# Performance work log

Measured on AMD Instinct MI355X. Metric: run time of the kernel, lower is better.

The kernel has to match this reference:

```python
import jax, jax.numpy as jnp
import numpy as np

N_NODES = 50000


def gcn_conv(h_in, W, b, src, dst, deg_inv_sqrt):
    """PyG GCNConv with self-loops and symmetric normalization.
    out_i = sum_{j->i} d_j^{-1/2} d_i^{-1/2} (h_j W) + d_i^{-1} (h_i W) + b
    """
    h = h_in @ W  # [N, out] transform first (efficient GCN form)
    norm = deg_inv_sqrt[src] * deg_inv_sqrt[dst]  # [E]
    msg = h[src] * norm[:, None]  # [E, out] edge gather
    agg = jax.ops.segment_sum(msg, dst, num_segments=N_NODES)
    # self-loop contribution with norm d_i^{-1/2} * d_i^{-1/2}
    agg = agg + h * (deg_inv_sqrt ** 2)[:, None]
    return agg + b


def setup_inputs() -> dict:
    key = jax.random.key(0)
    ks = jax.random.split(key, 8)
    n_input, n_hidden, n_latent = 512, 96, 32
    E = 800000
    x = jax.random.normal(ks[0], (N_NODES, n_input), dtype=jnp.float32)
    edge_index = jax.random.randint(ks[1], (2, E), 0, N_NODES, dtype=jnp.int64)
    s = 0.05
    W1 = jax.random.normal(ks[2], (n_input, n_hidden), dtype=jnp.float32) * s
    b1 = jnp.zeros((n_hidden,), dtype=jnp.float32)
    W_mu = jax.random.normal(ks[3], (n_hidden, n_latent), dtype=jnp.float32) * s
    b_mu = jnp.zeros((n_latent,), dtype=jnp.float32)
    W_logstd = jax.random.normal(ks[4], (n_hidden, n_latent), dtype=jnp.float32) * s
    b_logstd = jnp.zeros((n_latent,), dtype=jnp.float32)
    return {"x": x, "W1": W1, "b1": b1, "W_mu": W_mu, "b_mu": b_mu,
            "W_logstd": W_logstd, "b_logstd": b_logstd, "edge_index": edge_index}


def reference(x, W1, b1, W_mu, b_mu, W_logstd, b_logstd, edge_index):
    src, dst = edge_index[0], edge_index[1]
    # degree from targets with self-loops (PyG gcn_norm convention)
    deg = jax.ops.segment_sum(jnp.ones_like(dst, dtype=x.dtype), dst,
                              num_segments=N_NODES) + 1.0
    deg_inv_sqrt = jax.lax.rsqrt(deg)
    hidden = jax.nn.relu(gcn_conv(x, W1, b1, src, dst, deg_inv_sqrt))
    # dropout_rate = 0.0 -> identity
    mu = gcn_conv(hidden, W_mu, b_mu, src, dst, deg_inv_sqrt)
    logstd = gcn_conv(hidden, W_logstd, b_logstd, src, dst, deg_inv_sqrt)
    return (mu, logstd)
```

## Files before the change

### kernel.cpp

```cpp
#include <hip/hip_runtime.h>
#include <hip/hip_bf16.h>

#define N_NODES 50000
#define NIN 512
#define NH 96
#define NL 32
#define NH2 64

#define NB2 196
#define NBLK 128
#define BCAP 5120

typedef __attribute__((ext_vector_type(8))) short short8v;
typedef __attribute__((ext_vector_type(4))) float f32x4;

__device__ __forceinline__ unsigned short f2bf(float f) {
    __hip_bfloat16 h = __float2bfloat16(f);
    unsigned short u;
    __builtin_memcpy(&u, &h, 2);
    return u;
}
__device__ __forceinline__ float bf2f(unsigned short h) {
    return __uint_as_float((unsigned)h << 16);
}

__global__ __launch_bounds__(256) void k_prep(const float* __restrict__ W1,
                                              const float* __restrict__ Wmu,
                                              const float* __restrict__ Wls,
                                              unsigned short* __restrict__ WbT,
                                              unsigned short* __restrict__ W2T,
                                              int* __restrict__ gcur) {
    int idx = blockIdx.x * 256 + threadIdx.x;
    if (idx < NH * NIN) {
        int n = idx >> 9, k = idx & 511;
        WbT[idx] = f2bf(W1[(size_t)k * NH + n]);
    } else if (idx < NH * NIN + NH2 * NH) {
        int j = idx - NH * NIN;
        int n = j / NH, k = j - n * NH;
        float v = (n < NL) ? Wmu[k * NL + n] : Wls[k * NL + (n - NL)];
        W2T[j] = f2bf(v);
    }
    if (idx < NB2) gcur[idx] = 0;
}

__global__ __launch_bounds__(256) void k_coarse(const int* __restrict__ src,
                                                const int* __restrict__ dst,
                                                int* __restrict__ gcur,
                                                unsigned* __restrict__ cpair, int E) {
    __shared__ int hist[NB2];
    __shared__ int lpos[NB2];
    int t = threadIdx.x;
    int ch = (E + NBLK - 1) / NBLK;
    int e0 = blockIdx.x * ch, e1 = min(e0 + ch, E);
    for (int b = t; b < NB2; b += 256) hist[b] = 0;
    __syncthreads();
    for (int e = e0 + t; e < e1; e += 256)
        atomicAdd(&hist[dst[e] >> 8], 1);
    __syncthreads();
    for (int b = t; b < NB2; b += 256) {
        int cnt = hist[b];
        int base = (cnt > 0) ? atomicAdd(&gcur[b], cnt) : 0;
        lpos[b] = b * BCAP + base;
    }
    __syncthreads();
    for (int e = e0 + t; e < e1; e += 256) {
        int s = src[e], d = dst[e];
        int pos = atomicAdd(&lpos[d >> 8], 1);
        cpair[pos] = (unsigned)s | ((unsigned)d << 16);
    }
}

__global__ __launch_bounds__(256) void k_fine(const unsigned* __restrict__ cpair,
                                              const int* __restrict__ gcur,
                                              int* __restrict__ rowoff,
                                              float* __restrict__ dis,
                                              int* __restrict__ esrc) {
    __shared__ int lcnt[256];
    __shared__ int lscan[256];
    int bb = blockIdx.x;
    int n0 = bb << 8;
    int t = threadIdx.x;
    lscan[t] = (t < bb) ? gcur[t] : 0;
    __syncthreads();
    for (int off = 128; off > 0; off >>= 1) {
        if (t < off) lscan[t] += lscan[t + off];
        __syncthreads();
    }
    int base = lscan[0];
    if (bb == NB2 - 1 && t == 0) rowoff[N_NODES] = base + gcur[bb];
    lcnt[t] = 0;
    __syncthreads();
    int p0 = bb * BCAP;
    int p1 = p0 + gcur[bb];
    for (int p = p0 + t; p < p1; p += 256)
        atomicAdd(&lcnt[(cpair[p] >> 16) - n0], 1);
    __syncthreads();
    int cnt = lcnt[t];
    lscan[t] = cnt;
    __syncthreads();
    for (int off = 1; off < 256; off <<= 1) {
        int u = (t >= off) ? lscan[t - off] : 0;
        __syncthreads();
        lscan[t] += u;
        __syncthreads();
    }
    int excl = lscan[t] - cnt;
    int node = n0 + t;
    if (node < N_NODES) {
        rowoff[node] = base + excl;
        dis[node] = rsqrtf((float)cnt + 1.0f);
    }
    lcnt[t] = base + excl;
    __syncthreads();
    for (int p = p0 + t; p < p1; p += 256) {
        unsigned u = cpair[p];
        int d = (int)(u >> 16);
        int pos = atomicAdd(&lcnt[d - n0], 1);
        esrc[pos] = (int)(u & 0xFFFFu);
    }
}

#define GBM 64
__global__ __launch_bounds__(256, 3) void k_gemm1(const float* __restrict__ x,
                                                  const unsigned short* __restrict__ WbT,
                                                  const float* __restrict__ dis,
                                                  unsigned short* __restrict__ hb, int M) {
    __shared__ __align__(16) char lA[64 * 128];
    __shared__ __align__(16) char lB[96 * 128];
    int tid = threadIdx.x;
    int lane = tid & 63, w = tid >> 6;
    int l15 = lane & 15, hi = lane >> 4;
    int m0 = blockIdx.x * GBM;

    f32x4 acc[6];
#pragma unroll
    for (int nt = 0; nt < 6; ++nt)
#pragma unroll
        for (int i = 0; i < 4; ++i) acc[nt][i] = 0.f;

    int key = l15 & 7;
    int arow = (w * 16 + l15) * 128;

    for (int kt = 0; kt < 8; ++kt) {
        __syncthreads();
#pragma unroll
        for (int i = 0; i < 2; ++i) {
            int s = i * 256 + tid;
            int r = s >> 3, sl = s & 7;
            const float* p = x + (size_t)min(m0 + r, M - 1) * NIN + kt * 64 + sl * 8;
            float4 a0 = *reinterpret_cast<const float4*>(p);
            float4 a1 = *reinterpret_cast<const float4*>(p + 4);
            uint4 pk;
            pk.x = (unsigned)f2bf(a0.x) | ((unsigned)f2bf(a0.y) << 16);
            pk.y = (unsigned)f2bf(a0.z) | ((unsigned)f2bf(a0.w) << 16);
            pk.z = (unsigned)f2bf(a1.x) | ((unsigned)f2bf(a1.y) << 16);
            pk.w = (unsigned)f2bf(a1.z) | ((unsigned)f2bf(a1.w) << 16);
            *reinterpret_cast<uint4*>(lA + r * 128 + ((sl ^ (r & 7)) << 4)) = pk;
        }
#pragma unroll
        for (int i = 0; i < 3; ++i) {
            int s = i * 256 + tid;
            int n = s >> 3, sl = s & 7;
            uint4 bv = *reinterpret_cast<const uint4*>(WbT + (size_t)n * NIN + kt * 64 + sl * 8);
            *reinterpret_cast<uint4*>(lB + n * 128 + ((sl ^ (n & 7)) << 4)) = bv;
        }
        __syncthreads();

#pragma unroll
        for (int kc = 0; kc < 2; ++kc) {
            int off = (((kc * 4 + hi) ^ key) << 4);
            short8v a = *reinterpret_cast<const short8v*>(lA + arow + off);
#pragma unroll
            for (int nt = 0; nt < 6; ++nt) {
                short8v bv = *reinterpret_cast<const short8v*>(lB + (nt * 16 + l15) * 128 + off);
                acc[nt] = __builtin_amdgcn_mfma_f32_16x16x32_bf16(a, bv, acc[nt], 0, 0, 0);
            }
        }
    }

    int rbase = m0 + w * 16 + hi * 4;
#pragma unroll
    for (int r = 0; r < 4; ++r) {
        int orow = rbase + r;
        if (orow < M) {
            float dv = dis[orow];
            unsigned short* op = hb + (size_t)orow * NH + l15;
#pragma unroll
            for (int nt = 0; nt < 6; ++nt) op[nt * 16] = f2bf(acc[nt][r] * dv);
        }
    }
}

__global__ __launch_bounds__(256) void k_gather1(const ushort4* __restrict__ hb4,
                                                 const int* __restrict__ rowoff,
                                                 const int* __restrict__ esrc,
                                                 const float* __restrict__ dis,
                                                 const float* __restrict__ b1,
                                                 ushort4* __restrict__ hid4) {
    int tid = threadIdx.x;
    int node = blockIdx.x * 8 + (tid >> 5);
    int c = tid & 31;
    if (node >= N_NODES) return;
    int p0 = rowoff[node], p1 = rowoff[node + 1];
    bool act = (c < 24);
    float ax = 0.f, ay = 0.f, az = 0.f, aw = 0.f;
    for (int pb = p0; pb < p1; pb += 32) {
        int nb = min(32, p1 - pb);
        int sv = (c < nb) ? esrc[pb + c] : 0;
#pragma unroll 4
        for (int j = 0; j < nb; j++) {
            int s = __shfl(sv, j, 32);
            if (act) {
                ushort4 v = hb4[(size_t)s * 24 + c];
                ax += bf2f(v.x); ay += bf2f(v.y); az += bf2f(v.z); aw += bf2f(v.w);
            }
        }
    }
    if (act) {
        float dv = dis[node];
        ushort4 hv = hb4[(size_t)node * 24 + c];
        float4 bv = reinterpret_cast<const float4*>(b1)[c];
        ushort4 o;
        o.x = f2bf(fmaxf((ax + bf2f(hv.x)) * dv + bv.x, 0.f));
        o.y = f2bf(fmaxf((ay + bf2f(hv.y)) * dv + bv.y, 0.f));
        o.z = f2bf(fmaxf((az + bf2f(hv.z)) * dv + bv.z, 0.f));
        o.w = f2bf(fmaxf((aw + bf2f(hv.w)) * dv + bv.w, 0.f));
        hid4[(size_t)node * 24 + c] = o;
    }
}

#define GBM2 64
__global__ __launch_bounds__(256) void k_gemm2(const unsigned short* __restrict__ hid,
                                               const unsigned short* __restrict__ W2T,
                                               const float* __restrict__ dis,
                                               unsigned short* __restrict__ h23, int M) {
    __shared__ __align__(16) char lA[64 * 256];
    __shared__ __align__(16) char lB[64 * 256];
    int tid = threadIdx.x;
    int lane = tid & 63, w = tid >> 6;
    int l15 = lane & 15, hi = lane >> 4;
    int m0 = blockIdx.x * GBM2;

#pragma unroll
    for (int i = 0; i < 3; ++i) {
        int s = i * 256 + tid;
        int r = s / 12, sl = s - r * 12;
        uint4 v = *reinterpret_cast<const uint4*>(
            hid + (size_t)min(m0 + r, M - 1) * NH + sl * 8);
        *reinterpret_cast<uint4*>(lA + r * 256 + ((sl ^ (r & 7)) << 4)) = v;
    }
#pragma unroll
    for (int i = 0; i < 3; ++i) {
        int s = i * 256 + tid;
        int n = s / 12, sl = s - n * 12;
        uint4 v = *reinterpret_cast<const uint4*>(W2T + (size_t)n * NH + sl * 8);
        *reinterpret_cast<uint4*>(lB + n * 256 + ((sl ^ (n & 7)) << 4)) = v;
    }
    __syncthreads();

    f32x4 acc[4];
#pragma unroll
    for (int nt = 0; nt < 4; ++nt)
#pragma unroll
        for (int i = 0; i < 4; ++i) acc[nt][i] = 0.f;

    int key = l15 & 7;
    const char* aptr = lA + (w * 16 + l15) * 256;
#pragma unroll
    for (int kc = 0; kc < 3; ++kc) {
        int off = (((kc * 4 + hi) ^ key) << 4);
        short8v a = *reinterpret_cast<const short8v*>(aptr + off);
#pragma unroll
        for (int nt = 0; nt < 4; ++nt) {
            short8v bv = *reinterpret_cast<const short8v*>(lB + (nt * 16 + l15) * 256 + off);
            acc[nt] = __builtin_amdgcn_mfma_f32_16x16x32_bf16(a, bv, acc[nt], 0, 0, 0);
        }
    }

    int rbase = m0 + w * 16 + hi * 4;
#pragma unroll
    for (int r = 0; r < 4; ++r) {
        int orow = rbase + r;
        if (orow < M) {
            float dv = dis[orow];
            unsigned short* op = h23 + (size_t)orow * NH2 + l15;
#pragma unroll
            for (int nt = 0; nt < 4; ++nt) op[nt * 16] = f2bf(acc[nt][r] * dv);
        }
    }
}

__global__ __launch_bounds__(256) void k_gather2(const ushort4* __restrict__ hb4,
                                                 const int* __restrict__ rowoff,
                                                 const int* __restrict__ esrc,
                                                 const float* __restrict__ dis,
                                                 const float* __restrict__ bmu,
                                                 const float* __restrict__ bls,
                                                 float4* __restrict__ out4) {
    int tid = threadIdx.x;
    int node = blockIdx.x * 16 + (tid >> 4);
    int c = tid & 15;
    if (node >= N_NODES) return;
    int p0 = rowoff[node], p1 = rowoff[node + 1];
    float ax = 0.f, ay = 0.f, az = 0.f, aw = 0.f;
    for (int pb = p0; pb < p1; pb += 16) {
        int nb = min(16, p1 - pb);
        int sv = (c < nb) ? esrc[pb + c] : 0;
#pragma unroll 4
        for (int j = 0; j < nb; j++) {
            int s = __shfl(sv, j, 16);
            ushort4 v = hb4[(size_t)s * 16 + c];
            ax += bf2f(v.x); ay += bf2f(v.y); az += bf2f(v.z); aw += bf2f(v.w);
        }
    }
    float dv = dis[node];
    ushort4 hv = hb4[(size_t)node * 16 + c];
    float4 bv = (c < 8) ? reinterpret_cast<const float4*>(bmu)[c]
                        : reinterpret_cast<const float4*>(bls)[c - 8];
    float4 o;
    o.x = (ax + bf2f(hv.x)) * dv + bv.x;
    o.y = (ay + bf2f(hv.y)) * dv + bv.y;
    o.z = (az + bf2f(hv.z)) * dv + bv.z;
    o.w = (aw + bf2f(hv.w)) * dv + bv.w;
    if (c < 8) out4[(size_t)node * 8 + c] = o;
    else       out4[(size_t)N_NODES * 8 + (size_t)node * 8 + (c - 8)] = o;
}

extern "C" void kernel_launch(void* const* d_in, const int* in_sizes, int n_in,
                              void* d_out, int out_size, void* d_ws, size_t ws_size,
                              hipStream_t stream) {
    const float* x   = (const float*)d_in[0];
    const float* W1  = (const float*)d_in[1];
    const float* b1  = (const float*)d_in[2];
    const float* Wmu = (const float*)d_in[3];
    const float* bmu = (const float*)d_in[4];
    const float* Wls = (const float*)d_in[5];
    const float* bls = (const float*)d_in[6];
    const int*   ei  = (const int*)d_in[7];
    int E = in_sizes[7] / 2;
    const int* src  = ei;
    const int* dstp = ei + E;

    char* w = (char*)d_ws;
    int* rowoff  = (int*)w;            w += ((size_t)N_NODES + 4) * 4;
    float* dis   = (float*)w;          w += (size_t)N_NODES * 4;
    int* gcur    = (int*)w;            w += ((size_t)NB2 + 4) * 4;
    int* esrc    = (int*)w;            w += (size_t)E * 4;
    unsigned* cpair = (unsigned*)w;    w += (size_t)NB2 * BCAP * 4;
    unsigned short* WbT  = (unsigned short*)w;  w += (size_t)NH * NIN * 2;
    unsigned short* W2T  = (unsigned short*)w;  w += (size_t)NH2 * NH * 2;
    unsigned short* hbuf = (unsigned short*)w;  w += (size_t)N_NODES * NH * 2;
    unsigned short* hid  = (unsigned short*)w;  w += (size_t)N_NODES * NH * 2;
    unsigned short* h23  = (unsigned short*)w;  w += (size_t)N_NODES * NH2 * 2;

    int prep_n = NH * NIN + NH2 * NH;
    k_prep<<<(prep_n + 255) / 256, 256, 0, stream>>>(W1, Wmu, Wls, WbT, W2T, gcur);

    k_coarse<<<NBLK, 256, 0, stream>>>(src, dstp, gcur, cpair, E);
    k_fine<<<NB2, 256, 0, stream>>>(cpair, gcur, rowoff, dis, esrc);

    k_gemm1<<<(N_NODES + GBM - 1) / GBM, 256, 0, stream>>>(x, WbT, dis, hbuf, N_NODES);

    k_gather1<<<(N_NODES + 7) / 8, 256, 0, stream>>>(
        (const ushort4*)hbuf, rowoff, esrc, dis, b1, (ushort4*)hid);

    k_gemm2<<<(N_NODES + GBM2 - 1) / GBM2, 256, 0, stream>>>(hid, W2T, dis, h23, N_NODES);

    k_gather2<<<(N_NODES + 15) / 16, 256, 0, stream>>>(
        (const ushort4*)h23, rowoff, esrc, dis, bmu, bls, (float4*)d_out);
}
```

Before: 140.5 us.

## Widen gather loads to 16B, double GEMM1 K-tile, cache edges in LDS

Both gather kernels now load 8 bf16 values (uint4) per lane instead of 4, so fewer lanes serve each node and more nodes fit per block. GEMM1 processes K in 128-wide tiles over 4 iterations instead of 64-wide over 8, which halves the barrier count but doubles LDS use. The coarse bucketing kernel stages packed src/dst pairs in shared memory so the second pass does not re-read the edge arrays from global memory. These changes raise LDS pressure, which may lower occupancy in GEMM1 and k_coarse.

```diff
diff --git a/kernel.cpp b/kernel.cpp
--- a/kernel.cpp
+++ b/kernel.cpp
@@ -10,6 +10,7 @@
 #define NB2 196
 #define NBLK 128
 #define BCAP 5120
+#define ECH 6250
 
 typedef __attribute__((ext_vector_type(8))) short short8v;
 typedef __attribute__((ext_vector_type(4))) float f32x4;
@@ -20,6 +21,8 @@
     __builtin_memcpy(&u, &h, 2);
     return u;
 }
+__device__ __forceinline__ float bflo(unsigned u) { return __uint_as_float(u << 16); }
+__device__ __forceinline__ float bfhi(unsigned u) { return __uint_as_float(u & 0xFFFF0000u); }
 __device__ __forceinline__ float bf2f(unsigned short h) {
     return __uint_as_float((unsigned)h << 16);
 }
@@ -47,15 +50,20 @@
                                                 const int* __restrict__ dst,
                                                 int* __restrict__ gcur,
                                                 unsigned* __restrict__ cpair, int E) {
+    __shared__ unsigned epk[ECH];
     __shared__ int hist[NB2];
     __shared__ int lpos[NB2];
     int t = threadIdx.x;
     int ch = (E + NBLK - 1) / NBLK;
     int e0 = blockIdx.x * ch, e1 = min(e0 + ch, E);
+    int n = e1 - e0;
     for (int b = t; b < NB2; b += 256) hist[b] = 0;
     __syncthreads();
-    for (int e = e0 + t; e < e1; e += 256)
-        atomicAdd(&hist[dst[e] >> 8], 1);
+    for (int li = t; li < n; li += 256) {
+        int s = src[e0 + li], d = dst[e0 + li];
+        epk[li] = (unsigned)s | ((unsigned)d << 16);
+        atomicAdd(&hist[d >> 8], 1);
+    }
     __syncthreads();
     for (int b = t; b < NB2; b += 256) {
         int cnt = hist[b];
@@ -63,10 +71,10 @@
         lpos[b] = b * BCAP + base;
     }
     __syncthreads();
-    for (int e = e0 + t; e < e1; e += 256) {
-        int s = src[e], d = dst[e];
-        int pos = atomicAdd(&lpos[d >> 8], 1);
-        cpair[pos] = (unsigned)s | ((unsigned)d << 16);
+    for (int li = t; li < n; li += 256) {
+        unsigned u = epk[li];
+        int pos = atomicAdd(&lpos[u >> 24], 1);
+        cpair[pos] = u;
     }
 }
 
@@ -125,8 +133,8 @@
                                                   const unsigned short* __restrict__ WbT,
                                                   const float* __restrict__ dis,
                                                   unsigned short* __restrict__ hb, int M) {
-    __shared__ __align__(16) char lA[64 * 128];
-    __shared__ __align__(16) char lB[96 * 128];
+    __shared__ __align__(16) char lA[64 * 256];
+    __shared__ __align__(16) char lB[96 * 256];
     int tid = threadIdx.x;
     int lane = tid & 63, w = tid >> 6;
     int l15 = lane & 15, hi = lane >> 4;
@@ -139,15 +147,15 @@
         for (int i = 0; i < 4; ++i) acc[nt][i] = 0.f;
 
     int key = l15 & 7;
-    int arow = (w * 16 + l15) * 128;
-
-    for (int kt = 0; kt < 8; ++kt) {
+    int arow = (w * 16 + l15) * 256;
+
+    for (int kt = 0; kt < 4; ++kt) {
         __syncthreads();
 #pragma unroll
-        for (int i = 0; i < 2; ++i) {
+        for (int i = 0; i < 4; ++i) {
             int s = i * 256 + tid;
-            int r = s >> 3, sl = s & 7;
-            const float* p = x + (size_t)min(m0 + r, M - 1) * NIN + kt * 64 + sl * 8;
+            int r = s >> 4, sl = s & 15;
+            const float* p = x + (size_t)min(m0 + r, M - 1) * NIN + kt * 128 + sl * 8;
             float4 a0 = *reinterpret_cast<const float4*>(p);
             float4 a1 = *reinterpret_cast<const float4*>(p + 4);
             uint4 pk;
@@ -155,24 +163,24 @@
             pk.y = (unsigned)f2bf(a0.z) | ((unsigned)f2bf(a0.w) << 16);
             pk.z = (unsigned)f2bf(a1.x) | ((unsigned)f2bf(a1.y) << 16);
             pk.w = (unsigned)f2bf(a1.z) | ((unsigned)f2bf(a1.w) << 16);
-            *reinterpret_cast<uint4*>(lA + r * 128 + ((sl ^ (r & 7)) << 4)) = pk;
-        }
-#pragma unroll
-        for (int i = 0; i < 3; ++i) {
+            *reinterpret_cast<uint4*>(lA + r * 256 + ((sl ^ (r & 7)) << 4)) = pk;
+        }
+#pragma unroll
+        for (int i = 0; i < 6; ++i) {
             int s = i * 256 + tid;
-            int n = s >> 3, sl = s & 7;
-            uint4 bv = *reinterpret_cast<const uint4*>(WbT + (size_t)n * NIN + kt * 64 + sl * 8);
-            *reinterpret_cast<uint4*>(lB + n * 128 + ((sl ^ (n & 7)) << 4)) = bv;
+            int n = s >> 4, sl = s & 15;
+            uint4 bv = *reinterpret_cast<const uint4*>(WbT + (size_t)n * NIN + kt * 128 + sl * 8);
+            *reinterpret_cast<uint4*>(lB + n * 256 + ((sl ^ (n & 7)) << 4)) = bv;
         }
         __syncthreads();
 
 #pragma unroll
-        for (int kc = 0; kc < 2; ++kc) {
+        for (int kc = 0; kc < 4; ++kc) {
             int off = (((kc * 4 + hi) ^ key) << 4);
             short8v a = *reinterpret_cast<const short8v*>(lA + arow + off);
 #pragma unroll
             for (int nt = 0; nt < 6; ++nt) {
-                short8v bv = *reinterpret_cast<const short8v*>(lB + (nt * 16 + l15) * 128 + off);
+                short8v bv = *reinterpret_cast<const short8v*>(lB + (nt * 16 + l15) * 256 + off);
                 acc[nt] = __builtin_amdgcn_mfma_f32_16x16x32_bf16(a, bv, acc[nt], 0, 0, 0);
             }
         }
@@ -191,41 +199,54 @@
     }
 }
 
-__global__ __launch_bounds__(256) void k_gather1(const ushort4* __restrict__ hb4,
+__global__ __launch_bounds__(256) void k_gather1(const uint4* __restrict__ hb4,
                                                  const int* __restrict__ rowoff,
                                                  const int* __restrict__ esrc,
                                                  const float* __restrict__ dis,
                                                  const float* __restrict__ b1,
-                                                 ushort4* __restrict__ hid4) {
+                                                 uint4* __restrict__ hid4) {
     int tid = threadIdx.x;
-    int node = blockIdx.x * 8 + (tid >> 5);
-    int c = tid & 31;
+    int node = blockIdx.x * 16 + (tid >> 4);
+    int c = tid & 15;
     if (node >= N_NODES) return;
     int p0 = rowoff[node], p1 = rowoff[node + 1];
-    bool act = (c < 24);
-    float ax = 0.f, ay = 0.f, az = 0.f, aw = 0.f;
-    for (int pb = p0; pb < p1; pb += 32) {
-        int nb = min(32, p1 - pb);
+    bool act = (c < 12);
+    float a0 = 0.f, a1 = 0.f, a2 = 0.f, a3 = 0.f;
+    float a4 = 0.f, a5 = 0.f, a6 = 0.f, a7 = 0.f;
+    for (int pb = p0; pb < p1; pb += 16) {
+        int nb = min(16, p1 - pb);
         int sv = (c < nb) ? esrc[pb + c] : 0;
 #pragma unroll 4
         for (int j = 0; j < nb; j++) {
-            int s = __shfl(sv, j, 32);
+            int s = __shfl(sv, j, 16);
             if (act) {
-                ushort4 v = hb4[(size_t)s * 24 + c];
-                ax += bf2f(v.x); ay += bf2f(v.y); az += bf2f(v.z); aw += bf2f(v.w);
+                uint4 v = hb4[(size_t)s * 12 + c];
+                a0 += bflo(v.x); a1 += bfhi(v.x);
+                a2 += bflo(v.y); a3 += bfhi(v.y);
+                a4 += bflo(v.z); a5 += bfhi(v.z);
+                a6 += bflo(v.w); a7 += bfhi(v.w);
             }
         }
     }
     if (act) {
         float dv = dis[node];
-        ushort4 hv = hb4[(size_t)node * 24 + c];
-        float4 bv = reinterpret_cast<const float4*>(b1)[c];
-        ushort4 o;
-        o.x = f2bf(fmaxf((ax + bf2f(hv.x)) * dv + bv.x, 0.f));
-        o.y = f2bf(fmaxf((ay + bf2f(hv.y)) * dv + bv.y, 0.f));
-        o.z = f2bf(fmaxf((az + bf2f(hv.z)) * dv + bv.z, 0.f));
-        o.w = f2bf(fmaxf((aw + bf2f(hv.w)) * dv + bv.w, 0.f));
-        hid4[(size_t)node * 24 + c] = o;
+        uint4 hv = hb4[(size_t)node * 12 + c];
+        float4 b0 = reinterpret_cast<const float4*>(b1)[c * 2];
+        float4 b4 = reinterpret_cast<const float4*>(b1)[c * 2 + 1];
+        float r0 = fmaxf((a0 + bflo(hv.x)) * dv + b0.x, 0.f);
+        float r1 = fmaxf((a1 + bfhi(hv.x)) * dv + b0.y, 0.f);
+        float r2 = fmaxf((a2 + bflo(hv.y)) * dv + b0.z, 0.f);
+        float r3 = fmaxf((a3 + bfhi(hv.y)) * dv + b0.w, 0.f);
+        float r4 = fmaxf((a4 + bflo(hv.z)) * dv + b4.x, 0.f);
+        float r5 = fmaxf((a5 + bfhi(hv.z)) * dv + b4.y, 0.f);
+        float r6 = fmaxf((a6 + bflo(hv.w)) * dv + b4.z, 0.f);
+        float r7 = fmaxf((a7 + bfhi(hv.w)) * dv + b4.w, 0.f);
+        uint4 o;
+        o.x = (unsigned)f2bf(r0) | ((unsigned)f2bf(r1) << 16);
+        o.y = (unsigned)f2bf(r2) | ((unsigned)f2bf(r3) << 16);
+        o.z = (unsigned)f2bf(r4) | ((unsigned)f2bf(r5) << 16);
+        o.w = (unsigned)f2bf(r6) | ((unsigned)f2bf(r7) << 16);
+        hid4[(size_t)node * 12 + c] = o;
     }
 }
 
@@ -290,7 +311,7 @@
     }
 }
 
-__global__ __launch_bounds__(256) void k_gather2(const ushort4* __restrict__ hb4,
+__global__ __launch_bounds__(256) void k_gather2(const uint4* __restrict__ hb4,
                                                  const int* __restrict__ rowoff,
                                                  const int* __restrict__ esrc,
                                                  const float* __restrict__ dis,
@@ -298,32 +319,43 @@
                                                  const float* __restrict__ bls,
                                                  float4* __restrict__ out4) {
     int tid = threadIdx.x;
-    int node = blockIdx.x * 16 + (tid >> 4);
-    int c = tid & 15;
+    int node = blockIdx.x * 32 + (tid >> 3);
+    int c = tid & 7;
     if (node >= N_NODES) return;
     int p0 = rowoff[node], p1 = rowoff[node + 1];
-    float ax = 0.f, ay = 0.f, az = 0.f, aw = 0.f;
-    for (int pb = p0; pb < p1; pb += 16) {
-        int nb = min(16, p1 - pb);
+    float a0 = 0.f, a1 = 0.f, a2 = 0.f, a3 = 0.f;
+    float a4 = 0.f, a5 = 0.f, a6 = 0.f, a7 = 0.f;
+    for (int pb = p0; pb < p1; pb += 8) {
+        int nb = min(8, p1 - pb);
         int sv = (c < nb) ? esrc[pb + c] : 0;
 #pragma unroll 4
         for (int j = 0; j < nb; j++) {
-            int s = __shfl(sv, j, 16);
-            ushort4 v = hb4[(size_t)s * 16 + c];
-            ax += bf2f(v.x); ay += bf2f(v.y); az += bf2f(v.z); aw += bf2f(v.w);
+            int s = __shfl(sv, j, 8);
+            uint4 v = hb4[(size_t)s * 8 + c];
+            a0 += bflo(v.x); a1 += bfhi(v.x);
+            a2 += bflo(v.y); a3 += bfhi(v.y);
+            a4 += bflo(v.z); a5 += bfhi(v.z);
+            a6 += bflo(v.w); a7 += bfhi(v.w);
         }
     }
     float dv = dis[node];
-    ushort4 hv = hb4[(size_t)node * 16 + c];
-    float4 bv = (c < 8) ? reinterpret_cast<const float4*>(bmu)[c]
-                        : reinterpret_cast<const float4*>(bls)[c - 8];
-    float4 o;
-    o.x = (ax + bf2f(hv.x)) * dv + bv.x;
-    o.y = (ay + bf2f(hv.y)) * dv + bv.y;
-    o.z = (az + bf2f(hv.z)) * dv + bv.z;
-    o.w = (aw + bf2f(hv.w)) * dv + bv.w;
-    if (c < 8) out4[(size_t)node * 8 + c] = o;
-    else       out4[(size_t)N_NODES * 8 + (size_t)node * 8 + (c - 8)] = o;
+    uint4 hv = hb4[(size_t)node * 8 + c];
+    const float4* bp = (c < 4) ? reinterpret_cast<const float4*>(bmu) + c * 2
+                               : reinterpret_cast<const float4*>(bls) + (c - 4) * 2;
+    float4 b0 = bp[0], b4 = bp[1];
+    float4 o0, o1;
+    o0.x = (a0 + bflo(hv.x)) * dv + b0.x;
+    o0.y = (a1 + bfhi(hv.x)) * dv + b0.y;
+    o0.z = (a2 + bflo(hv.y)) * dv + b0.z;
+    o0.w = (a3 + bfhi(hv.y)) * dv + b0.w;
+    o1.x = (a4 + bflo(hv.z)) * dv + b4.x;
+    o1.y = (a5 + bfhi(hv.z)) * dv + b4.y;
+    o1.z = (a6 + bflo(hv.w)) * dv + b4.z;
+    o1.w = (a7 + bfhi(hv.w)) * dv + b4.w;
+    size_t base = (c < 4) ? (size_t)node * 8 + c * 2
+                          : (size_t)N_NODES * 8 + (size_t)node * 8 + (c - 4) * 2;
+    out4[base] = o0;
+    out4[base + 1] = o1;
 }
 
 extern "C" void kernel_launch(void* const* d_in, const int* in_sizes, int n_in,
@@ -361,11 +393,11 @@
 
     k_gemm1<<<(N_NODES + GBM - 1) / GBM, 256, 0, stream>>>(x, WbT, dis, hbuf, N_NODES);
 
-    k_gather1<<<(N_NODES + 7) / 8, 256, 0, stream>>>(
-        (const ushort4*)hbuf, rowoff, esrc, dis, b1, (ushort4*)hid);
+    k_gather1<<<(N_NODES + 15) / 16, 256, 0, stream>>>(
+        (const uint4*)hbuf, rowoff, esrc, dis, b1, (uint4*)hid);
 
     k_gemm2<<<(N_NODES + GBM2 - 1) / GBM2, 256, 0, stream>>>(hid, W2T, dis, h23, N_NODES);
 
-    k_gather2<<<(N_NODES + 15) / 16, 256, 0, stream>>>(
-        (const ushort4*)h23, rowoff, esrc, dis, bmu, bls, (float4*)d_out);
-}
+    k_gather2<<<(N_NODES + 31) / 32, 256, 0, stream>>>(
+        (const uint4*)h23, rowoff, esrc, dis, bmu, bls, (float4*)d_out);
+}
```

New measurement: 120.6 us. -14.2%, faster.
